# Kernel tuning notes

Hardware: AMD Instinct MI355X
Metric: run time of the kernel (lower is better)

Reference implementation:

```python
import jax, jax.numpy as jnp
import numpy as np

N_NODES = 50000; N_INTRA = 800000; N_INTER = 400000; N_IEDGE = 600000
N_GRAPHS = 128; F_IN = 54; DIM = 128; N_GNN = 3; DIM_MLP = 128
DEV_VDW_COEFF = 0.2; EPS_LO = 0.0178; EPS_HI = 0.2
VDW_N_SHORT = 10.0; VDW_N_LONG = 6.0
RANGE_LO = 0.5; RANGE_HI = 5.0
HBOND_CUT = (-0.7, 0.0); METAL_CUT = (-0.7, 0.0); HYDRO_CUT = (0.5, 1.5)


def _lin(key, fi, fo):
    return jax.random.normal(key, (fi, fo), jnp.float32) / np.float32(np.sqrt(fi))


def setup_inputs():
    key = jax.random.key(0)
    ks = iter(jax.random.split(key, 48))
    nk = lambda: next(ks)
    inp = {}
    inp['x'] = jax.random.normal(nk(), (N_NODES, F_IN), jnp.float32)
    inp['pos'] = jax.random.uniform(nk(), (N_NODES, 3), jnp.float32, 0.0, 20.0)
    inp['vdw_radii'] = jax.random.uniform(nk(), (N_NODES,), jnp.float32, 1.0, 2.0)
    inp['rotor'] = jax.random.randint(nk(), (N_GRAPHS, 1), 0, 20).astype(jnp.float32)
    inp['edge_index'] = jax.random.randint(nk(), (2, N_INTRA), 0, N_NODES)
    inp['edge_index_c'] = jax.random.randint(nk(), (2, N_INTER), 0, N_NODES)
    inp['edge_index_i'] = jax.random.randint(nk(), (2, N_IEDGE), 0, N_NODES)
    inp['batch'] = jnp.sort(jax.random.randint(nk(), (N_NODES,), 0, N_GRAPHS))
    for name, p in (('is_metal', 0.02), ('is_h_donor', 0.15), ('is_h_acceptor', 0.2), ('is_hydrophobic', 0.4)):
        inp[name] = jax.random.bernoulli(nk(), p, (N_NODES,))
    inp['embed_W'] = _lin(nk(), F_IN, DIM)
    inp['gat_W'] = jax.random.normal(nk(), (N_GNN, DIM, DIM), jnp.float32) / np.float32(np.sqrt(DIM))
    inp['gat_Wb'] = jnp.zeros((N_GNN, DIM), jnp.float32)
    inp['gat_A'] = 0.1 * jax.random.normal(nk(), (N_GNN, DIM, DIM), jnp.float32) / np.float32(np.sqrt(DIM))
    inp['gat_gate_w'] = jax.random.normal(nk(), (N_GNN, 2 * DIM, 1), jnp.float32) / np.float32(np.sqrt(2 * DIM))
    inp['gat_gate_b'] = jnp.zeros((N_GNN, 1), jnp.float32)
    inp['inter_W'] = jax.random.normal(nk(), (N_GNN, DIM, DIM), jnp.float32) / np.float32(np.sqrt(DIM))
    inp['inter_Wb'] = jnp.zeros((N_GNN, DIM), jnp.float32)
    inp['inter_gate_w'] = jax.random.normal(nk(), (N_GNN, 2 * DIM, 1), jnp.float32) / np.float32(np.sqrt(2 * DIM))
    inp['inter_gate_b'] = jnp.zeros((N_GNN, 1), jnp.float32)
    inp['eps_w1'] = _lin(nk(), 2 * DIM, DIM_MLP); inp['eps_b1'] = jnp.zeros((DIM_MLP,), jnp.float32)
    inp['eps_w2'] = _lin(nk(), DIM_MLP, 1); inp['eps_b2'] = jnp.zeros((1,), jnp.float32)
    inp['dvdw_w1'] = _lin(nk(), 2 * DIM, DIM_MLP); inp['dvdw_b1'] = jnp.zeros((DIM_MLP,), jnp.float32)
    inp['dvdw_w2'] = _lin(nk(), DIM_MLP, 1); inp['dvdw_b2'] = jnp.zeros((1,), jnp.float32)
    inp['hbond_coeff'] = jnp.array([1.0], jnp.float32)
    inp['hydrophobic_coeff'] = jnp.array([0.5], jnp.float32)
    inp['rotor_coeff'] = jnp.array([0.5], jnp.float32)
    return inp


def _gated_gat(x, src, dst, W, Wb, A, gw, gb):
    n = x.shape[0]
    h = x @ W + Wb                                   # [N, D]
    logits = jnp.sum((h @ A)[dst] * h[src], axis=-1)  # per-edge attention logit
    mx = jax.ops.segment_max(logits, dst, num_segments=n)
    mx = jnp.where(jnp.isfinite(mx), mx, 0.0)
    ex = jnp.exp(logits - mx[dst])
    den = jax.ops.segment_sum(ex, dst, num_segments=n)
    alpha = ex / (den[dst] + 1e-16)                  # segment softmax over incoming edges
    h_prime = jax.nn.relu(jax.ops.segment_sum(alpha[:, None] * h[src], dst, num_segments=n))
    z = jax.nn.sigmoid(jnp.concatenate([x, h_prime], -1) @ gw + gb)
    return z * x + (1.0 - z) * h_prime


def _interaction(x, src, dst, W, Wb, gw, gb):
    n = x.shape[0]
    m = jax.ops.segment_sum(jax.nn.relu(x[src] @ W + Wb), dst, num_segments=n)
    z = jax.nn.sigmoid(jnp.concatenate([x, m], -1) @ gw + gb)
    return z * x + (1.0 - z) * m


def _lj(D, R, eps, n_short, n_long):
    dr = jnp.maximum(D / R, 0.5)  # numerical clamp mirroring PIGNet's distance clamp
    n = jnp.where(dr < 1.0, n_short, n_long)
    return eps * (dr ** (-2.0 * n) - 2.0 * dr ** (-n))


def _linear_potential(D, R, minima, c_short, c_long):
    frac = jnp.clip(((D - R) - c_long) / (c_short - c_long), 0.0, 1.0)
    return minima * frac


def _forward(x, pos, vdw_radii, rotor, embed_W, gat_W, gat_Wb, gat_A, gat_gate_w, gat_gate_b,
             inter_W, inter_Wb, inter_gate_w, inter_gate_b,
             eps_w1, eps_b1, eps_w2, eps_b2, dvdw_w1, dvdw_b1, dvdw_w2, dvdw_b2,
             hbond_coeff, hydrophobic_coeff, rotor_coeff,
             edge_index, edge_index_c, edge_index_i, batch,
             is_metal, is_h_donor, is_h_acceptor, is_hydrophobic):
    h = x @ embed_W
    for l in range(N_GNN):
        h = _gated_gat(h, edge_index[0], edge_index[1], gat_W[l], gat_Wb[l], gat_A[l], gat_gate_w[l], gat_gate_b[l])
    for l in range(N_GNN):
        h = _interaction(h, edge_index_c[0], edge_index_c[1], inter_W[l], inter_Wb[l], inter_gate_w[l], inter_gate_b[l])
    i, j = edge_index_i[0], edge_index_i[1]
    diff = pos[i] - pos[j]
    D = jnp.sqrt(jnp.sum(diff * diff, axis=-1) + 1e-10)           # [E]
    rmask = ((D >= RANGE_LO) & (D <= RANGE_HI)).astype(h.dtype)
    x_cat = jnp.concatenate([h[i], h[j]], axis=-1)                # [E, 2*DIM]
    dvdw = jnp.tanh(jax.nn.relu(x_cat @ dvdw_w1 + dvdw_b1) @ dvdw_w2 + dvdw_b2)[:, 0]
    dvdw = dvdw * DEV_VDW_COEFF * rmask
    R = vdw_radii[i] + vdw_radii[j] + dvdw
    eps = jax.nn.sigmoid(jax.nn.relu(x_cat @ eps_w1 + eps_b1) @ eps_w2 + eps_b2)[:, 0]
    eps = eps * (EPS_HI - EPS_LO) + EPS_LO
    min_hb = -hbond_coeff ** 2
    min_hp = -hydrophobic_coeff ** 2
    e = jnp.stack([
        _lj(D, R, eps, VDW_N_SHORT, VDW_N_LONG),
        _linear_potential(D, R, min_hb, *HBOND_CUT),
        _linear_potential(D, R, min_hb, *METAL_CUT),
        _linear_potential(D, R, min_hp, *HYDRO_CUT),
    ])                                                            # [4, E]
    no_metal = ~(is_metal[i] | is_metal[j])
    masks = jnp.stack([
        no_metal,
        ((is_h_donor[i] & is_h_acceptor[j]) | (is_h_acceptor[i] & is_h_donor[j])) & no_metal,
        (is_metal[i] & is_h_acceptor[j]) | (is_h_acceptor[i] & is_metal[j]),
        is_hydrophobic[i] & is_hydrophobic[j] & no_metal,
    ]).astype(e.dtype)
    e = e * masks * rmask
    energies = jax.ops.segment_sum(e.T, batch[i], num_segments=N_GRAPHS)  # [G, 4]
    penalty = 1.0 + rotor_coeff ** 2 * rotor                               # [G, 1]
    return energies / penalty, dvdw


def reference(x, pos, vdw_radii, rotor, edge_index, edge_index_c, edge_index_i, batch,
              is_metal, is_h_donor, is_h_acceptor, is_hydrophobic,
              embed_W, gat_W, gat_Wb, gat_A, gat_gate_w, gat_gate_b,
              inter_W, inter_Wb, inter_gate_w, inter_gate_b,
              eps_w1, eps_b1, eps_w2, eps_b2, dvdw_w1, dvdw_b1, dvdw_w2, dvdw_b2,
              hbond_coeff, hydrophobic_coeff, rotor_coeff):
    return _forward(x, pos, vdw_radii, rotor, embed_W, gat_W, gat_Wb, gat_A, gat_gate_w, gat_gate_b,
                    inter_W, inter_Wb, inter_gate_w, inter_gate_b,
                    eps_w1, eps_b1, eps_w2, eps_b2, dvdw_w1, dvdw_b1, dvdw_w2, dvdw_b2,
                    hbond_coeff, hydrophobic_coeff, rotor_coeff,
                    edge_index, edge_index_c, edge_index_i, batch,
                    is_metal, is_h_donor, is_h_acceptor, is_hydrophobic)
```

## Files before the change

### kernel.cpp

```cpp
#include <hip/hip_runtime.h>
#include <math.h>

#define NN 50000
#define EA 800000
#define EC 400000
#define EIN 600000
#define NG 128
#define FIN 54

#define DEV_VDW 0.2f
#define EPS_LO_ 0.0178f
#define EPS_HI_ 0.2f

typedef unsigned int uint;
typedef unsigned short ushort;
typedef __attribute__((ext_vector_type(8))) short bf16x8;
typedef __attribute__((ext_vector_type(4))) float f32x4;

__device__ __forceinline__ ushort f2bf(float f){
  uint x = __float_as_uint(f);
  uint r = x + 0x7fffu + ((x >> 16) & 1u);
  return (ushort)(r >> 16);
}
__device__ __forceinline__ uint f2bf2(float a, float b){
  return (uint)f2bf(a) | ((uint)f2bf(b) << 16);
}
__device__ __forceinline__ float2 bf2x2(uint u){
  return make_float2(__uint_as_float(u << 16), __uint_as_float(u & 0xffff0000u));
}
__device__ __forceinline__ void decode8(uint4 u, float* f){
  f[0] = __uint_as_float(u.x << 16); f[1] = __uint_as_float(u.x & 0xffff0000u);
  f[2] = __uint_as_float(u.y << 16); f[3] = __uint_as_float(u.y & 0xffff0000u);
  f[4] = __uint_as_float(u.z << 16); f[5] = __uint_as_float(u.z & 0xffff0000u);
  f[6] = __uint_as_float(u.w << 16); f[7] = __uint_as_float(u.w & 0xffff0000u);
}

__global__ void k_count(const int* __restrict__ dst, int E, int* __restrict__ cnt){
  int i = blockIdx.x * blockDim.x + threadIdx.x;
  int stride = gridDim.x * blockDim.x;
  for (; i < E; i += stride) atomicAdd(&cnt[dst[i]], 1);
}

__global__ void k_scan(const int* __restrict__ cnt, int n, int* __restrict__ off, int* __restrict__ cur){
  __shared__ int wsums[16];
  __shared__ int run_s;
  int tid = threadIdx.x;
  int lane = tid & 63, w = tid >> 6;
  if (tid == 0) run_s = 0;
  __syncthreads();
  for (int base = 0; base < n; base += 1024){
    int run = run_s;
    int i = base + tid;
    int v = (i < n) ? cnt[i] : 0;
    int s = v;
    #pragma unroll
    for (int o = 1; o < 64; o <<= 1){ int t = __shfl_up(s, o, 64); if (lane >= o) s += t; }
    if (lane == 63) wsums[w] = s;
    __syncthreads();
    if (w == 0 && lane < 16){
      int t = wsums[lane];
      #pragma unroll
      for (int o = 1; o < 16; o <<= 1){ int u = __shfl_up(t, o, 64); if (lane >= o) t += u; }
      wsums[lane] = t;
    }
    __syncthreads();
    int woff = (w == 0) ? 0 : wsums[w - 1];
    int excl = run + woff + (s - v);
    if (i < n){ off[i] = excl; cur[i] = excl; }
    int tot = wsums[15];
    __syncthreads();
    if (tid == 0) run_s = run + tot;
    __syncthreads();
  }
  if (threadIdx.x == 0) off[n] = run_s;
}

__global__ void k_place(const int* __restrict__ src, const int* __restrict__ dst, int E,
                        int* __restrict__ cur, int* __restrict__ out_src){
  int i = blockIdx.x * blockDim.x + threadIdx.x;
  int stride = gridDim.x * blockDim.x;
  for (; i < E; i += stride){
    int d = dst[i];
    int slot = atomicAdd(&cur[d], 1);
    out_src[slot] = src[i];
  }
}

__global__ void k_nodeinfo(const float* __restrict__ POS, const float* __restrict__ RAD,
                           const int* __restrict__ Mmet, const int* __restrict__ Mdon,
                           const int* __restrict__ Macc, const int* __restrict__ Mhyd,
                           const int* __restrict__ BATCH,
                           float4* __restrict__ PRAD, uint* __restrict__ MB){
  int n = blockIdx.x * 256 + threadIdx.x;
  if (n < NN){
    PRAD[n] = make_float4(POS[3*n], POS[3*n+1], POS[3*n+2], RAD[n]);
    uint m = (Mmet[n] ? 1u : 0u) | (Mdon[n] ? 2u : 0u) | (Macc[n] ? 4u : 0u) |
             (Mhyd[n] ? 8u : 0u) | ((uint)BATCH[n] << 8);
    MB[n] = m;
  }
}

__global__ __launch_bounds__(256) void k_prepw(const float* __restrict__ gatW, const float* __restrict__ gatA,
                        const float* __restrict__ intW, const float* __restrict__ dw1,
                        const float* __restrict__ ew1, const float* __restrict__ db1,
                        const float* __restrict__ eb1,
                        uint* __restrict__ Wt, float* __restrict__ BIASB){
  __shared__ ushort L[128 * 130];
  int m = blockIdx.x;
  int tid = threadIdx.x;
  if (m == 13){
    if (tid < 512){
      int c = tid & 127, y = tid >> 7;
      float v = (y == 0) ? db1[c] : (y == 2) ? eb1[c] : 0.f;
      BIASB[tid] = v;
    }
    if (tid < 128) BIASB[512 + tid] = 0.f;
    return;
  }
  const float* src = (m < 3)  ? gatW + m * 16384 :
                     (m < 6)  ? gatA + (m - 3) * 16384 :
                     (m < 9)  ? intW + (m - 6) * 16384 :
                     (m < 11) ? dw1 + (m - 9) * 16384 :
                                ew1 + (m - 11) * 16384;
  for (int idx = tid; idx < 16384; idx += 256){
    int k = idx >> 7, n = idx & 127;
    L[k * 130 + n] = f2bf(src[idx]);
  }
  __syncthreads();
  int n = tid & 127, half = tid >> 7;
  uint* outp = Wt + (size_t)m * 8192 + n * 64 + half * 32;
  #pragma unroll
  for (int kk2 = 0; kk2 < 32; ++kk2){
    int k = half * 64 + 2 * kk2;
    uint u = (uint)L[k * 130 + n] | ((uint)L[(k + 1) * 130 + n] << 16);
    outp[kk2] = u;
  }
}

__global__ void k_embed(const float* __restrict__ X, const float* __restrict__ W,
                        float* __restrict__ H, uint* __restrict__ Hh){
  __shared__ float Wls[FIN * 128];
  int tid = threadIdx.x;
  for (int i = tid; i < FIN * 128; i += 128) Wls[i] = W[i];
  __syncthreads();
  for (int row = blockIdx.x; row < NN; row += gridDim.x){
    const float* xr = X + row * FIN;
    float acc = 0.f;
    #pragma unroll
    for (int k = 0; k < FIN; ++k) acc += xr[k] * Wls[k * 128 + tid];
    H[(size_t)row * 128 + tid] = acc;
    ((ushort*)Hh)[(size_t)row * 128 + tid] = f2bf(acc);
  }
}

template<bool RELU>
__global__ __launch_bounds__(256) void k_gemm_mfma(const uint* __restrict__ Ah,
        const uint* __restrict__ Bt0, const float* __restrict__ bias0,
        uint* __restrict__ C0, size_t strideC, int N){
  const uint* Bt = Bt0 + (size_t)blockIdx.y * 8192;
  const float* bias = bias0 + (size_t)blockIdx.y * 128;
  uint* Cout = C0 + (size_t)blockIdx.y * strideC;
  int tid = threadIdx.x;
  int lane = tid & 63;
  int wv = tid >> 6;
  int row0 = blockIdx.x * 128 + wv * 32;
  int l15 = lane & 15, lg = lane >> 4;
  int ra0 = row0 + l15, ra1 = row0 + 16 + l15;
  const uint* pa0 = Ah + (size_t)(ra0 < N ? ra0 : 0) * 64 + lg * 4;
  const uint* pa1 = Ah + (size_t)(ra1 < N ? ra1 : 0) * 64 + lg * 4;
  const uint* pb  = Bt + (size_t)l15 * 64 + lg * 4;
  f32x4 acc[2][8] = {};
  #pragma unroll
  for (int c = 0; c < 4; ++c){
    bf16x8 a0 = *(const bf16x8*)(pa0 + c * 16);
    bf16x8 a1 = *(const bf16x8*)(pa1 + c * 16);
    #pragma unroll
    for (int ct = 0; ct < 8; ++ct){
      bf16x8 b = *(const bf16x8*)(pb + ct * 1024 + c * 16);
      acc[0][ct] = __builtin_amdgcn_mfma_f32_16x16x32_bf16(a0, b, acc[0][ct], 0, 0, 0);
      acc[1][ct] = __builtin_amdgcn_mfma_f32_16x16x32_bf16(a1, b, acc[1][ct], 0, 0, 0);
    }
  }
  #pragma unroll
  for (int ct = 0; ct < 8; ++ct){
    int col = ct * 16 + l15;
    float bv = bias[col];
    #pragma unroll
    for (int rt = 0; rt < 2; ++rt){
      int rbase = row0 + rt * 16 + lg * 4;
      f32x4 a4 = acc[rt][ct];
      #pragma unroll
      for (int r = 0; r < 4; ++r){
        int row = rbase + r;
        if (row < N){
          float t = a4[r] + bv;
          if (RELU) t = fmaxf(t, 0.f);
          ((ushort*)Cout)[(size_t)row * 128 + col] = f2bf(t);
        }
      }
    }
  }
}

__global__ __launch_bounds__(256) void k_gat(float* __restrict__ H, uint* __restrict__ Hh,
                      const uint* __restrict__ HWh, const uint* __restrict__ HAh,
                      const int* __restrict__ off, const int* __restrict__ srcs,
                      const float* __restrict__ GW, const float* __restrict__ GB){
  int tid = threadIdx.x;
  int sub = tid & 15;
  int n = blockIdx.x * 16 + (tid >> 4);
  if (n >= NN) return;
  uint4 au = *(const uint4*)(HAh + (size_t)n * 64 + sub * 4);
  float a[8]; decode8(au, a);
  int e0 = off[n], deg = off[n + 1] - e0;
  float m = -INFINITY, den = 0.f;
  float acc[8] = {};
  uint4 wu = {};
  if (deg > 0){
    int s = srcs[e0];
    wu = *(const uint4*)(HWh + (size_t)s * 64 + sub * 4);
  }
  for (int t = 0; t < deg; ++t){
    uint4 wnow = wu;
    if (t + 1 < deg){
      int s2 = srcs[e0 + t + 1];
      wu = *(const uint4*)(HWh + (size_t)s2 * 64 + sub * 4);
    }
    float w[8]; decode8(wnow, w);
    float p = a[0]*w[0] + a[1]*w[1] + a[2]*w[2] + a[3]*w[3]
            + a[4]*w[4] + a[5]*w[5] + a[6]*w[6] + a[7]*w[7];
    #pragma unroll
    for (int o = 8; o; o >>= 1) p += __shfl_xor(p, o, 64);
    float mn = fmaxf(m, p);
    float cf = __expf(m - mn);
    float ex = __expf(p - mn);
    den = den * cf + ex;
    #pragma unroll
    for (int q = 0; q < 8; ++q) acc[q] = acc[q] * cf + ex * w[q];
    m = mn;
  }
  float inv = 1.f / (den + 1e-16f);
  float hp[8];
  #pragma unroll
  for (int q = 0; q < 8; ++q) hp[q] = fmaxf(acc[q] * inv, 0.f);
  float x[8];
  *(float4*)&x[0] = *(const float4*)(H + (size_t)n * 128 + sub * 8);
  *(float4*)&x[4] = *(const float4*)(H + (size_t)n * 128 + sub * 8 + 4);
  float gx[8], gh[8];
  *(float4*)&gx[0] = *(const float4*)(GW + sub * 8);
  *(float4*)&gx[4] = *(const float4*)(GW + sub * 8 + 4);
  *(float4*)&gh[0] = *(const float4*)(GW + 128 + sub * 8);
  *(float4*)&gh[4] = *(const float4*)(GW + 128 + sub * 8 + 4);
  float g = 0.f;
  #pragma unroll
  for (int q = 0; q < 8; ++q) g += x[q] * gx[q] + hp[q] * gh[q];
  #pragma unroll
  for (int o = 8; o; o >>= 1) g += __shfl_xor(g, o, 64);
  g += GB[0];
  float z = 1.f / (1.f + __expf(-g));
  #pragma unroll
  for (int q = 0; q < 8; ++q) x[q] = z * x[q] + (1.f - z) * hp[q];
  *(float4*)(H + (size_t)n * 128 + sub * 8)     = *(float4*)&x[0];
  *(float4*)(H + (size_t)n * 128 + sub * 8 + 4) = *(float4*)&x[4];
  uint4 hw;
  hw.x = f2bf2(x[0], x[1]); hw.y = f2bf2(x[2], x[3]);
  hw.z = f2bf2(x[4], x[5]); hw.w = f2bf2(x[6], x[7]);
  *(uint4*)(Hh + (size_t)n * 64 + sub * 4) = hw;
}

__global__ __launch_bounds__(256) void k_inter(float* __restrict__ H, uint* __restrict__ Hh,
                        const uint* __restrict__ Th,
                        const int* __restrict__ off, const int* __restrict__ srcs,
                        const float* __restrict__ GW, const float* __restrict__ GB){
  int tid = threadIdx.x;
  int sub = tid & 15;
  int n = blockIdx.x * 16 + (tid >> 4);
  if (n >= NN) return;
  int e0 = off[n], deg = off[n + 1] - e0;
  float acc[8] = {};
  uint4 wu = {};
  if (deg > 0){
    int s = srcs[e0];
    wu = *(const uint4*)(Th + (size_t)s * 64 + sub * 4);
  }
  for (int t = 0; t < deg; ++t){
    uint4 wnow = wu;
    if (t + 1 < deg){
      int s2 = srcs[e0 + t + 1];
      wu = *(const uint4*)(Th + (size_t)s2 * 64 + sub * 4);
    }
    float w[8]; decode8(wnow, w);
    #pragma unroll
    for (int q = 0; q < 8; ++q) acc[q] += w[q];
  }
  float x[8];
  *(float4*)&x[0] = *(const float4*)(H + (size_t)n * 128 + sub * 8);
  *(float4*)&x[4] = *(const float4*)(H + (size_t)n * 128 + sub * 8 + 4);
  float gx[8], gh[8];
  *(float4*)&gx[0] = *(const float4*)(GW + sub * 8);
  *(float4*)&gx[4] = *(const float4*)(GW + sub * 8 + 4);
  *(float4*)&gh[0] = *(const float4*)(GW + 128 + sub * 8);
  *(float4*)&gh[4] = *(const float4*)(GW + 128 + sub * 8 + 4);
  float g = 0.f;
  #pragma unroll
  for (int q = 0; q < 8; ++q) g += x[q] * gx[q] + acc[q] * gh[q];
  #pragma unroll
  for (int o = 8; o; o >>= 1) g += __shfl_xor(g, o, 64);
  g += GB[0];
  float z = 1.f / (1.f + __expf(-g));
  #pragma unroll
  for (int q = 0; q < 8; ++q) x[q] = z * x[q] + (1.f - z) * acc[q];
  *(float4*)(H + (size_t)n * 128 + sub * 8)     = *(float4*)&x[0];
  *(float4*)(H + (size_t)n * 128 + sub * 8 + 4) = *(float4*)&x[4];
  uint4 hw;
  hw.x = f2bf2(x[0], x[1]); hw.y = f2bf2(x[2], x[3]);
  hw.z = f2bf2(x[4], x[5]); hw.w = f2bf2(x[6], x[7]);
  *(uint4*)(Hh + (size_t)n * 64 + sub * 4) = hw;
}

__global__ __launch_bounds__(256) void k_edges(
    const int* __restrict__ EI,
    const float4* __restrict__ PRAD, const uint* __restrict__ MB,
    const uint* __restrict__ Pd, const uint* __restrict__ Qd,
    const uint* __restrict__ Pe, const uint* __restrict__ Qe,
    const float* __restrict__ w2d, const float* __restrict__ b2d,
    const float* __restrict__ w2e, const float* __restrict__ b2e,
    const float* __restrict__ hbc, const float* __restrict__ hpc,
    float* __restrict__ geng, float* __restrict__ outdv){
  __shared__ float eg[NG * 4];
  int tid = threadIdx.x;
  for (int i = tid; i < NG * 4; i += 256) eg[i] = 0.f;
  __syncthreads();
  int sub = tid & 15;
  int gid = blockIdx.x * 16 + (tid >> 4);
  int ngrp = gridDim.x * 16;
  float wdv[8], wev[8];
  *(float4*)&wdv[0] = *(const float4*)(w2d + sub * 8);
  *(float4*)&wdv[4] = *(const float4*)(w2d + sub * 8 + 4);
  *(float4*)&wev[0] = *(const float4*)(w2e + sub * 8);
  *(float4*)&wev[4] = *(const float4*)(w2e + sub * 8 + 4);
  float bd = b2d[0], be = b2e[0];
  float minhb = -hbc[0] * hbc[0], minhp = -hpc[0] * hpc[0];

  int e = gid;
  uint4 pd0 = {}, qd0 = {}, pe0 = {}, qe0 = {};
  float4 pri0 = {}, prj0 = {};
  uint mbi0 = 0, mbj0 = 0;
  int i1 = 0, j1 = 0;
  if (e < EIN){
    int i0 = EI[e], j0 = EI[EIN + e];
    pd0 = *(const uint4*)(Pd + (size_t)i0 * 64 + sub * 4);
    qd0 = *(const uint4*)(Qd + (size_t)j0 * 64 + sub * 4);
    pe0 = *(const uint4*)(Pe + (size_t)i0 * 64 + sub * 4);
    qe0 = *(const uint4*)(Qe + (size_t)j0 * 64 + sub * 4);
    pri0 = PRAD[i0]; prj0 = PRAD[j0]; mbi0 = MB[i0]; mbj0 = MB[j0];
  }
  if (e + ngrp < EIN){ i1 = EI[e + ngrp]; j1 = EI[EIN + e + ngrp]; }

  for (; e < EIN; e += ngrp){
    uint4 pd1 = {}, qd1 = {}, pe1 = {}, qe1 = {};
    float4 pri1 = {}, prj1 = {};
    uint mbi1 = 0, mbj1 = 0;
    int i2 = 0, j2 = 0;
    if (e + ngrp < EIN){
      pd1 = *(const uint4*)(Pd + (size_t)i1 * 64 + sub * 4);
      qd1 = *(const uint4*)(Qd + (size_t)j1 * 64 + sub * 4);
      pe1 = *(const uint4*)(Pe + (size_t)i1 * 64 + sub * 4);
      qe1 = *(const uint4*)(Qe + (size_t)j1 * 64 + sub * 4);
      pri1 = PRAD[i1]; prj1 = PRAD[j1]; mbi1 = MB[i1]; mbj1 = MB[j1];
    }
    if (e + 2 * ngrp < EIN){ i2 = EI[e + 2 * ngrp]; j2 = EI[EIN + e + 2 * ngrp]; }

    float pdf[8], qdf[8], pef[8], qef[8];
    decode8(pd0, pdf); decode8(qd0, qdf); decode8(pe0, pef); decode8(qe0, qef);
    float sd = 0.f, se = 0.f;
    #pragma unroll
    for (int q = 0; q < 8; ++q){
      sd += fmaxf(pdf[q] + qdf[q], 0.f) * wdv[q];
      se += fmaxf(pef[q] + qef[q], 0.f) * wev[q];
    }
    #pragma unroll
    for (int o = 8; o; o >>= 1){
      sd += __shfl_xor(sd, o, 64);
      se += __shfl_xor(se, o, 64);
    }
    sd += bd; se += be;
    float dx = pri0.x - prj0.x, dy = pri0.y - prj0.y, dz = pri0.z - prj0.z;
    float D = sqrtf(dx * dx + dy * dy + dz * dz + 1e-10f);
    float rmask = (D >= 0.5f && D <= 5.0f) ? 1.f : 0.f;
    float dvdw = tanhf(sd) * DEV_VDW * rmask;
    float eps = (1.f / (1.f + __expf(-se))) * (EPS_HI_ - EPS_LO_) + EPS_LO_;
    float R = pri0.w + prj0.w + dvdw;
    float dr = fmaxf(D / R, 0.5f);
    float nn2 = (dr < 1.f) ? 10.f : 6.f;
    float tp = __expf(-nn2 * __logf(dr));
    float ev = eps * (tp * tp - 2.f * tp);
    float dmr = D - R;
    float f1 = fminf(fmaxf(dmr * (-1.f / 0.7f), 0.f), 1.f);
    float f3 = fminf(fmaxf(1.5f - dmr, 0.f), 1.f);
    bool metI = mbi0 & 1, metJ = mbj0 & 1;
    bool donI = mbi0 & 2, donJ = mbj0 & 2;
    bool accI = mbi0 & 4, accJ = mbj0 & 4;
    bool hyI  = mbi0 & 8, hyJ  = mbj0 & 8;
    bool nm = !(metI || metJ);
    float E0 = nm ? ev * rmask : 0.f;
    float E1 = (((donI && accJ) || (accI && donJ)) && nm) ? minhb * f1 * rmask : 0.f;
    float E2 = ((metI && accJ) || (accI && metJ)) ? minhb * f1 * rmask : 0.f;
    float E3 = (hyI && hyJ && nm) ? minhp * f3 * rmask : 0.f;
    if (sub == 0){
      outdv[e] = dvdw;
      int g = (int)(mbi0 >> 8) * 4;
      atomicAdd(&eg[g + 0], E0);
      atomicAdd(&eg[g + 1], E1);
      atomicAdd(&eg[g + 2], E2);
      atomicAdd(&eg[g + 3], E3);
    }
    pd0 = pd1; qd0 = qd1; pe0 = pe1; qe0 = qe1;
    pri0 = pri1; prj0 = prj1; mbi0 = mbi1; mbj0 = mbj1;
    i1 = i2; j1 = j2;
  }
  __syncthreads();
  float* part = geng + (size_t)(blockIdx.x & 7) * (NG * 4);
  for (int i2 = tid; i2 < NG * 4; i2 += 256) atomicAdd(&part[i2], eg[i2]);
}

__global__ void k_final(const float* __restrict__ geng, const float* __restrict__ rotor,
                        const float* __restrict__ rc, float* __restrict__ out){
  int t = blockIdx.x * blockDim.x + threadIdx.x;
  if (t < NG * 4){
    int g = t >> 2;
    float s = 0.f;
    #pragma unroll
    for (int p = 0; p < 8; ++p) s += geng[p * NG * 4 + t];
    float pen = 1.f + rc[0] * rc[0] * rotor[g];
    out[t] = s / pen;
  }
}

extern "C" void kernel_launch(void* const* d_in, const int* in_sizes, int n_in,
                              void* d_out, int out_size, void* d_ws, size_t ws_size,
                              hipStream_t stream){
  (void)in_sizes; (void)n_in; (void)out_size; (void)ws_size;
  const float* X    = (const float*)d_in[0];
  const float* POS  = (const float*)d_in[1];
  const float* RAD  = (const float*)d_in[2];
  const float* ROT  = (const float*)d_in[3];
  const int* EIa    = (const int*)d_in[4];
  const int* EIc    = (const int*)d_in[5];
  const int* EIi    = (const int*)d_in[6];
  const int* BATCH  = (const int*)d_in[7];
  const int* Mmet = (const int*)d_in[8];
  const int* Mdon = (const int*)d_in[9];
  const int* Macc = (const int*)d_in[10];
  const int* Mhyd = (const int*)d_in[11];
  const float* embW  = (const float*)d_in[12];
  const float* gatW  = (const float*)d_in[13];
  const float* gatWb = (const float*)d_in[14];
  const float* gatA  = (const float*)d_in[15];
  const float* gatGw = (const float*)d_in[16];
  const float* gatGb = (const float*)d_in[17];
  const float* intW  = (const float*)d_in[18];
  const float* intWb = (const float*)d_in[19];
  const float* intGw = (const float*)d_in[20];
  const float* intGb = (const float*)d_in[21];
  const float* ew1 = (const float*)d_in[22];
  const float* eb1 = (const float*)d_in[23];
  const float* ew2 = (const float*)d_in[24];
  const float* eb2 = (const float*)d_in[25];
  const float* dw1 = (const float*)d_in[26];
  const float* db1 = (const float*)d_in[27];
  const float* dw2 = (const float*)d_in[28];
  const float* db2 = (const float*)d_in[29];
  const float* hbc = (const float*)d_in[30];
  const float* hpc = (const float*)d_in[31];
  const float* rcc = (const float*)d_in[32];
  float* out = (float*)d_out;

  char* w = (char*)d_ws;
  float* H   = (float*)w; w += (size_t)NN * 128 * 4;
  uint* Hh   = (uint*)w;  w += (size_t)NN * 64 * 4;
  uint* BAh  = (uint*)w;  w += (size_t)NN * 64 * 4;
  uint* BBh  = (uint*)w;  w += (size_t)NN * 64 * 4;
  uint* Peh  = (uint*)w;  w += (size_t)NN * 64 * 4;
  uint* Qeh  = (uint*)w;  w += (size_t)NN * 64 * 4;
  uint* WT   = (uint*)w;  w += (size_t)13 * 8192 * 4;
  float* BIASB = (float*)w; w += 640 * 4;
  float4* PRAD = (float4*)w; w += (size_t)NN * 16;
  uint* MBb  = (uint*)w;  w += (size_t)NN * 4;
  float* GENG = (float*)w; w += (size_t)8 * 512 * 4;
  int* cntA = (int*)w; w += (size_t)NN * 4;
  int* offA = (int*)w; w += (size_t)(NN + 1) * 4;
  int* curA = (int*)w; w += (size_t)NN * 4;
  int* srcA = (int*)w; w += (size_t)EA * 4;
  int* cntC = (int*)w; w += (size_t)NN * 4;
  int* offC = (int*)w; w += (size_t)(NN + 1) * 4;
  int* curC = (int*)w; w += (size_t)NN * 4;
  int* srcC = (int*)w; w += (size_t)EC * 4;
  uint* Th  = BAh;
  uint* Pdh = BAh;
  uint* Qdh = BBh;
  const float* zeros128 = BIASB + 512;

  hipMemsetAsync(cntA, 0, (size_t)NN * 4, stream);
  hipMemsetAsync(cntC, 0, (size_t)NN * 4, stream);
  hipMemsetAsync(GENG, 0, (size_t)8 * 512 * 4, stream);

  k_count<<<1024, 256, 0, stream>>>(EIa + EA, EA, cntA);
  k_scan<<<1, 1024, 0, stream>>>(cntA, NN, offA, curA);
  k_place<<<1024, 256, 0, stream>>>(EIa, EIa + EA, EA, curA, srcA);
  k_count<<<1024, 256, 0, stream>>>(EIc + EC, EC, cntC);
  k_scan<<<1, 1024, 0, stream>>>(cntC, NN, offC, curC);
  k_place<<<1024, 256, 0, stream>>>(EIc, EIc + EC, EC, curC, srcC);

  k_prepw<<<14, 256, 0, stream>>>(gatW, gatA, intW, dw1, ew1, db1, eb1, WT, BIASB);
  k_nodeinfo<<<(NN + 255) / 256, 256, 0, stream>>>(POS, RAD, Mmet, Mdon, Macc, Mhyd, BATCH, PRAD, MBb);
  k_embed<<<2048, 128, 0, stream>>>(X, embW, H, Hh);

  int gg = (NN + 127) / 128;
  int nodeGrid = (NN + 15) / 16;
  for (int l = 0; l < 3; ++l){
    k_gemm_mfma<false><<<dim3(gg, 1), 256, 0, stream>>>(Hh,  WT + (size_t)l * 8192,       gatWb + l * 128, BAh, 0, NN);
    k_gemm_mfma<false><<<dim3(gg, 1), 256, 0, stream>>>(BAh, WT + (size_t)(3 + l) * 8192, zeros128,        BBh, 0, NN);
    k_gat<<<nodeGrid, 256, 0, stream>>>(H, Hh, BAh, BBh, offA, srcA, gatGw + l * 256, gatGb + l);
  }
  for (int l = 0; l < 3; ++l){
    k_gemm_mfma<true><<<dim3(gg, 1), 256, 0, stream>>>(Hh, WT + (size_t)(6 + l) * 8192, intWb + l * 128, Th, 0, NN);
    k_inter<<<nodeGrid, 256, 0, stream>>>(H, Hh, Th, offC, srcC, intGw + l * 256, intGb + l);
  }
  k_gemm_mfma<false><<<dim3(gg, 4), 256, 0, stream>>>(Hh, WT + (size_t)9 * 8192, BIASB, BAh, (size_t)NN * 64, NN);

  k_edges<<<2048, 256, 0, stream>>>(EIi, PRAD, MBb, Pdh, Qdh, Peh, Qeh,
                                    dw2, db2, ew2, eb2, hbc, hpc,
                                    GENG, out + 512);
  k_final<<<2, 256, 0, stream>>>(GENG, ROT, rcc, out);
}
```

Measured before the change: 852.8 us.

## Precompose GAT weight products, split neighbor loops across lanes, merge CSR builds

Several changes at once. The GAT attention matrix is folded into the layer weight at prep time (A' = W·A, plus bias·A), so the two chained GEMMs per layer become a single GEMM launch with two outputs. The GAT and inter aggregation kernels now use a 64-lane wave per node, with four lane groups each taking every fourth neighbor; the partial online-softmax results and the sums are merged with shuffles, which adds parallelism for memory-latency-bound gathers. The A and C CSR count/scan/place kernels are merged into single launches, and the edge kernel uses fast tanh and division intrinsics. The precomposed weight is rounded to bf16 after the product rather than before the second GEMM, which changes numerics slightly.

```diff
diff --git a/kernel.cpp b/kernel.cpp
--- a/kernel.cpp
+++ b/kernel.cpp
@@ -25,9 +25,6 @@
 __device__ __forceinline__ uint f2bf2(float a, float b){
   return (uint)f2bf(a) | ((uint)f2bf(b) << 16);
 }
-__device__ __forceinline__ float2 bf2x2(uint u){
-  return make_float2(__uint_as_float(u << 16), __uint_as_float(u & 0xffff0000u));
-}
 __device__ __forceinline__ void decode8(uint4 u, float* f){
   f[0] = __uint_as_float(u.x << 16); f[1] = __uint_as_float(u.x & 0xffff0000u);
   f[2] = __uint_as_float(u.y << 16); f[3] = __uint_as_float(u.y & 0xffff0000u);
@@ -35,13 +32,23 @@
   f[6] = __uint_as_float(u.w << 16); f[7] = __uint_as_float(u.w & 0xffff0000u);
 }
 
-__global__ void k_count(const int* __restrict__ dst, int E, int* __restrict__ cnt){
-  int i = blockIdx.x * blockDim.x + threadIdx.x;
-  int stride = gridDim.x * blockDim.x;
-  for (; i < E; i += stride) atomicAdd(&cnt[dst[i]], 1);
-}
-
-__global__ void k_scan(const int* __restrict__ cnt, int n, int* __restrict__ off, int* __restrict__ cur){
+__global__ void k_count2(const int* __restrict__ dstA, const int* __restrict__ dstC,
+                         int* __restrict__ cntA, int* __restrict__ cntC){
+  int half = blockIdx.x >= 1024;
+  const int* dst = half ? dstC : dstA;
+  int* cnt = half ? cntC : cntA;
+  int E = half ? EC : EA;
+  int bid = blockIdx.x - (half ? 1024 : 0);
+  int i = bid * 256 + threadIdx.x;
+  for (; i < E; i += 1024 * 256) atomicAdd(&cnt[dst[i]], 1);
+}
+
+__global__ void k_scan2(const int* __restrict__ cntA, int* __restrict__ offA, int* __restrict__ curA,
+                        const int* __restrict__ cntC, int* __restrict__ offC, int* __restrict__ curC){
+  const int* cnt = blockIdx.x ? cntC : cntA;
+  int* off = blockIdx.x ? offC : offA;
+  int* cur = blockIdx.x ? curC : curA;
+  int n = NN;
   __shared__ int wsums[16];
   __shared__ int run_s;
   int tid = threadIdx.x;
@@ -75,14 +82,21 @@
   if (threadIdx.x == 0) off[n] = run_s;
 }
 
-__global__ void k_place(const int* __restrict__ src, const int* __restrict__ dst, int E,
-                        int* __restrict__ cur, int* __restrict__ out_src){
-  int i = blockIdx.x * blockDim.x + threadIdx.x;
-  int stride = gridDim.x * blockDim.x;
-  for (; i < E; i += stride){
+__global__ void k_place2(const int* __restrict__ eiA, const int* __restrict__ eiC,
+                         int* __restrict__ curA, int* __restrict__ srcA,
+                         int* __restrict__ curC, int* __restrict__ srcC){
+  int half = blockIdx.x >= 1024;
+  const int* src = half ? eiC : eiA;
+  const int* dst = half ? eiC + EC : eiA + EA;
+  int* cur = half ? curC : curA;
+  int* outp = half ? srcC : srcA;
+  int E = half ? EC : EA;
+  int bid = blockIdx.x - (half ? 1024 : 0);
+  int i = bid * 256 + threadIdx.x;
+  for (; i < E; i += 1024 * 256){
     int d = dst[i];
     int slot = atomicAdd(&cur[d], 1);
-    out_src[slot] = src[i];
+    outp[slot] = src[i];
   }
 }
 
@@ -102,29 +116,75 @@
 
 __global__ __launch_bounds__(256) void k_prepw(const float* __restrict__ gatW, const float* __restrict__ gatA,
                         const float* __restrict__ intW, const float* __restrict__ dw1,
-                        const float* __restrict__ ew1, const float* __restrict__ db1,
-                        const float* __restrict__ eb1,
-                        uint* __restrict__ Wt, float* __restrict__ BIASB){
-  __shared__ ushort L[128 * 130];
+                        const float* __restrict__ ew1,
+                        const float* __restrict__ gatWb, const float* __restrict__ intWb,
+                        const float* __restrict__ db1, const float* __restrict__ eb1,
+                        uint* __restrict__ Wt, float* __restrict__ BIASALL){
+  __shared__ ushort L[128 * 132];
   int m = blockIdx.x;
   int tid = threadIdx.x;
   if (m == 13){
-    if (tid < 512){
-      int c = tid & 127, y = tid >> 7;
-      float v = (y == 0) ? db1[c] : (y == 2) ? eb1[c] : 0.f;
-      BIASB[tid] = v;
-    }
-    if (tid < 128) BIASB[512 + tid] = 0.f;
+    for (int idx = tid; idx < 13 * 128; idx += 256){
+      int slot = idx >> 7, c = idx & 127;
+      if (slot >= 3 && slot < 6) continue;
+      float v = 0.f;
+      if (slot < 3) v = gatWb[slot * 128 + c];
+      else if (slot < 9) v = intWb[(slot - 6) * 128 + c];
+      else if (slot == 9) v = db1[c];
+      else if (slot == 11) v = eb1[c];
+      BIASALL[idx] = v;
+    }
     return;
   }
+  if (m >= 3 && m < 6){
+    int l = m - 3;
+    const float* Wf  = gatW + l * 16384;
+    const float* Af  = gatA + l * 16384;
+    const float* Wbf = gatWb + l * 128;
+    for (int idx = tid; idx < 16384; idx += 256){
+      int k = idx >> 7, n = idx & 127;
+      L[k * 132 + n] = f2bf(Af[idx]);
+    }
+    __syncthreads();
+    int r = tid >> 1, ch = tid & 1;
+    float accv[64];
+    #pragma unroll
+    for (int c = 0; c < 64; ++c) accv[c] = 0.f;
+    float accb = 0.f;
+    int bc = tid & 127;
+    for (int mm = 0; mm < 128; ++mm){
+      float wv = Wf[r * 128 + mm];
+      const uint* Lr32 = (const uint*)&L[mm * 132 + ch * 64];
+      #pragma unroll
+      for (int c2 = 0; c2 < 32; ++c2){
+        uint u = Lr32[c2];
+        accv[2 * c2]     += wv * __uint_as_float(u << 16);
+        accv[2 * c2 + 1] += wv * __uint_as_float(u & 0xffff0000u);
+      }
+      accb += Wbf[mm] * __uint_as_float((uint)L[mm * 132 + bc] << 16);
+    }
+    __syncthreads();
+    #pragma unroll
+    for (int c = 0; c < 64; ++c) L[r * 132 + ch * 64 + c] = f2bf(accv[c]);
+    if (tid < 128) BIASALL[(3 + l) * 128 + tid] = accb;
+    __syncthreads();
+    int n = tid & 127, half = tid >> 7;
+    uint* outp = Wt + (size_t)m * 8192 + n * 64 + half * 32;
+    #pragma unroll
+    for (int kk2 = 0; kk2 < 32; ++kk2){
+      int k = half * 64 + 2 * kk2;
+      uint u = (uint)L[k * 132 + n] | ((uint)L[(k + 1) * 132 + n] << 16);
+      outp[kk2] = u;
+    }
+    return;
+  }
   const float* src = (m < 3)  ? gatW + m * 16384 :
-                     (m < 6)  ? gatA + (m - 3) * 16384 :
                      (m < 9)  ? intW + (m - 6) * 16384 :
                      (m < 11) ? dw1 + (m - 9) * 16384 :
                                 ew1 + (m - 11) * 16384;
   for (int idx = tid; idx < 16384; idx += 256){
     int k = idx >> 7, n = idx & 127;
-    L[k * 130 + n] = f2bf(src[idx]);
+    L[k * 132 + n] = f2bf(src[idx]);
   }
   __syncthreads();
   int n = tid & 127, half = tid >> 7;
@@ -132,7 +192,7 @@
   #pragma unroll
   for (int kk2 = 0; kk2 < 32; ++kk2){
     int k = half * 64 + 2 * kk2;
-    uint u = (uint)L[k * 130 + n] | ((uint)L[(k + 1) * 130 + n] << 16);
+    uint u = (uint)L[k * 132 + n] | ((uint)L[(k + 1) * 132 + n] << 16);
     outp[kk2] = u;
   }
 }
@@ -155,10 +215,11 @@
 
 template<bool RELU>
 __global__ __launch_bounds__(256) void k_gemm_mfma(const uint* __restrict__ Ah,
-        const uint* __restrict__ Bt0, const float* __restrict__ bias0,
+        const uint* __restrict__ Bt0, size_t strideB,
+        const float* __restrict__ bias0, size_t strideBias,
         uint* __restrict__ C0, size_t strideC, int N){
-  const uint* Bt = Bt0 + (size_t)blockIdx.y * 8192;
-  const float* bias = bias0 + (size_t)blockIdx.y * 128;
+  const uint* Bt = Bt0 + (size_t)blockIdx.y * strideB;
+  const float* bias = bias0 + (size_t)blockIdx.y * strideBias;
   uint* Cout = C0 + (size_t)blockIdx.y * strideC;
   int tid = threadIdx.x;
   int lane = tid & 63;
@@ -207,36 +268,58 @@
                       const int* __restrict__ off, const int* __restrict__ srcs,
                       const float* __restrict__ GW, const float* __restrict__ GB){
   int tid = threadIdx.x;
-  int sub = tid & 15;
-  int n = blockIdx.x * 16 + (tid >> 4);
+  int n = blockIdx.x * 4 + (tid >> 6);
   if (n >= NN) return;
+  int lane = tid & 63;
+  int sub = lane & 15;
+  int grp = lane >> 4;
   uint4 au = *(const uint4*)(HAh + (size_t)n * 64 + sub * 4);
   float a[8]; decode8(au, a);
   int e0 = off[n], deg = off[n + 1] - e0;
-  float m = -INFINITY, den = 0.f;
+  float m = -1e30f, den = 0.f;
   float acc[8] = {};
+  int slot = grp;
+  bool act = slot < deg;
+  int sv = (sub == 0 && act) ? srcs[e0 + slot] : 0;
+  int s = __shfl(sv, lane & 48);
   uint4 wu = {};
-  if (deg > 0){
-    int s = srcs[e0];
-    wu = *(const uint4*)(HWh + (size_t)s * 64 + sub * 4);
-  }
-  for (int t = 0; t < deg; ++t){
-    uint4 wnow = wu;
-    if (t + 1 < deg){
-      int s2 = srcs[e0 + t + 1];
-      wu = *(const uint4*)(HWh + (size_t)s2 * 64 + sub * 4);
-    }
-    float w[8]; decode8(wnow, w);
+  if (act) wu = *(const uint4*)(HWh + (size_t)s * 64 + sub * 4);
+  int nit = (deg + 3) >> 2;
+  for (int t = 0; t < nit; ++t){
+    int slotn = slot + 4;
+    bool actn = slotn < deg;
+    int svn = (sub == 0 && actn) ? srcs[e0 + slotn] : 0;
+    int sn = __shfl(svn, lane & 48);
+    uint4 wun = {};
+    if (actn) wun = *(const uint4*)(HWh + (size_t)sn * 64 + sub * 4);
+    float w[8]; decode8(wu, w);
     float p = a[0]*w[0] + a[1]*w[1] + a[2]*w[2] + a[3]*w[3]
             + a[4]*w[4] + a[5]*w[5] + a[6]*w[6] + a[7]*w[7];
     #pragma unroll
     for (int o = 8; o; o >>= 1) p += __shfl_xor(p, o, 64);
-    float mn = fmaxf(m, p);
-    float cf = __expf(m - mn);
-    float ex = __expf(p - mn);
-    den = den * cf + ex;
-    #pragma unroll
-    for (int q = 0; q < 8; ++q) acc[q] = acc[q] * cf + ex * w[q];
+    if (act){
+      float mn = fmaxf(m, p);
+      float cf = __expf(m - mn);
+      float ex = __expf(p - mn);
+      den = den * cf + ex;
+      #pragma unroll
+      for (int q = 0; q < 8; ++q) acc[q] = acc[q] * cf + ex * w[q];
+      m = mn;
+    }
+    slot = slotn; act = actn; wu = wun;
+  }
+  #pragma unroll
+  for (int o = 16; o <= 32; o <<= 1){
+    float mo  = __shfl_xor(m, o, 64);
+    float dno = __shfl_xor(den, o, 64);
+    float ao[8];
+    #pragma unroll
+    for (int q = 0; q < 8; ++q) ao[q] = __shfl_xor(acc[q], o, 64);
+    float mn = fmaxf(m, mo);
+    float cf = __expf(m - mn), cfo = __expf(mo - mn);
+    den = den * cf + dno * cfo;
+    #pragma unroll
+    for (int q = 0; q < 8; ++q) acc[q] = acc[q] * cf + ao[q] * cfo;
     m = mn;
   }
   float inv = 1.f / (den + 1e-16f);
@@ -260,12 +343,14 @@
   float z = 1.f / (1.f + __expf(-g));
   #pragma unroll
   for (int q = 0; q < 8; ++q) x[q] = z * x[q] + (1.f - z) * hp[q];
-  *(float4*)(H + (size_t)n * 128 + sub * 8)     = *(float4*)&x[0];
-  *(float4*)(H + (size_t)n * 128 + sub * 8 + 4) = *(float4*)&x[4];
-  uint4 hw;
-  hw.x = f2bf2(x[0], x[1]); hw.y = f2bf2(x[2], x[3]);
-  hw.z = f2bf2(x[4], x[5]); hw.w = f2bf2(x[6], x[7]);
-  *(uint4*)(Hh + (size_t)n * 64 + sub * 4) = hw;
+  if (grp == 0){
+    *(float4*)(H + (size_t)n * 128 + sub * 8)     = *(float4*)&x[0];
+    *(float4*)(H + (size_t)n * 128 + sub * 8 + 4) = *(float4*)&x[4];
+    uint4 hw;
+    hw.x = f2bf2(x[0], x[1]); hw.y = f2bf2(x[2], x[3]);
+    hw.z = f2bf2(x[4], x[5]); hw.w = f2bf2(x[6], x[7]);
+    *(uint4*)(Hh + (size_t)n * 64 + sub * 4) = hw;
+  }
 }
 
 __global__ __launch_bounds__(256) void k_inter(float* __restrict__ H, uint* __restrict__ Hh,
@@ -273,25 +358,38 @@
                         const int* __restrict__ off, const int* __restrict__ srcs,
                         const float* __restrict__ GW, const float* __restrict__ GB){
   int tid = threadIdx.x;
-  int sub = tid & 15;
-  int n = blockIdx.x * 16 + (tid >> 4);
+  int n = blockIdx.x * 4 + (tid >> 6);
   if (n >= NN) return;
+  int lane = tid & 63;
+  int sub = lane & 15;
+  int grp = lane >> 4;
   int e0 = off[n], deg = off[n + 1] - e0;
   float acc[8] = {};
+  int slot = grp;
+  bool act = slot < deg;
+  int sv = (sub == 0 && act) ? srcs[e0 + slot] : 0;
+  int s = __shfl(sv, lane & 48);
   uint4 wu = {};
-  if (deg > 0){
-    int s = srcs[e0];
-    wu = *(const uint4*)(Th + (size_t)s * 64 + sub * 4);
-  }
-  for (int t = 0; t < deg; ++t){
-    uint4 wnow = wu;
-    if (t + 1 < deg){
-      int s2 = srcs[e0 + t + 1];
-      wu = *(const uint4*)(Th + (size_t)s2 * 64 + sub * 4);
-    }
-    float w[8]; decode8(wnow, w);
-    #pragma unroll
-    for (int q = 0; q < 8; ++q) acc[q] += w[q];
+  if (act) wu = *(const uint4*)(Th + (size_t)s * 64 + sub * 4);
+  int nit = (deg + 3) >> 2;
+  for (int t = 0; t < nit; ++t){
+    int slotn = slot + 4;
+    bool actn = slotn < deg;
+    int svn = (sub == 0 && actn) ? srcs[e0 + slotn] : 0;
+    int sn = __shfl(svn, lane & 48);
+    uint4 wun = {};
+    if (actn) wun = *(const uint4*)(Th + (size_t)sn * 64 + sub * 4);
+    if (act){
+      float w[8]; decode8(wu, w);
+      #pragma unroll
+      for (int q = 0; q < 8; ++q) acc[q] += w[q];
+    }
+    slot = slotn; act = actn; wu = wun;
+  }
+  #pragma unroll
+  for (int q = 0; q < 8; ++q){
+    acc[q] += __shfl_xor(acc[q], 16, 64);
+    acc[q] += __shfl_xor(acc[q], 32, 64);
   }
   float x[8];
   *(float4*)&x[0] = *(const float4*)(H + (size_t)n * 128 + sub * 8);
@@ -310,12 +408,14 @@
   float z = 1.f / (1.f + __expf(-g));
   #pragma unroll
   for (int q = 0; q < 8; ++q) x[q] = z * x[q] + (1.f - z) * acc[q];
-  *(float4*)(H + (size_t)n * 128 + sub * 8)     = *(float4*)&x[0];
-  *(float4*)(H + (size_t)n * 128 + sub * 8 + 4) = *(float4*)&x[4];
-  uint4 hw;
-  hw.x = f2bf2(x[0], x[1]); hw.y = f2bf2(x[2], x[3]);
-  hw.z = f2bf2(x[4], x[5]); hw.w = f2bf2(x[6], x[7]);
-  *(uint4*)(Hh + (size_t)n * 64 + sub * 4) = hw;
+  if (grp == 0){
+    *(float4*)(H + (size_t)n * 128 + sub * 8)     = *(float4*)&x[0];
+    *(float4*)(H + (size_t)n * 128 + sub * 8 + 4) = *(float4*)&x[4];
+    uint4 hw;
+    hw.x = f2bf2(x[0], x[1]); hw.y = f2bf2(x[2], x[3]);
+    hw.z = f2bf2(x[4], x[5]); hw.w = f2bf2(x[6], x[7]);
+    *(uint4*)(Hh + (size_t)n * 64 + sub * 4) = hw;
+  }
 }
 
 __global__ __launch_bounds__(256) void k_edges(
@@ -388,10 +488,12 @@
     float dx = pri0.x - prj0.x, dy = pri0.y - prj0.y, dz = pri0.z - prj0.z;
     float D = sqrtf(dx * dx + dy * dy + dz * dz + 1e-10f);
     float rmask = (D >= 0.5f && D <= 5.0f) ? 1.f : 0.f;
-    float dvdw = tanhf(sd) * DEV_VDW * rmask;
-    float eps = (1.f / (1.f + __expf(-se))) * (EPS_HI_ - EPS_LO_) + EPS_LO_;
+    float ex2 = __expf(2.f * fminf(sd, 15.f));
+    float th = __fdividef(ex2 - 1.f, ex2 + 1.f);
+    float dvdw = th * DEV_VDW * rmask;
+    float eps = __fdividef(1.f, 1.f + __expf(-se)) * (EPS_HI_ - EPS_LO_) + EPS_LO_;
     float R = pri0.w + prj0.w + dvdw;
-    float dr = fmaxf(D / R, 0.5f);
+    float dr = fmaxf(__fdividef(D, R), 0.5f);
     float nn2 = (dr < 1.f) ? 10.f : 6.f;
     float tp = __expf(-nn2 * __logf(dr));
     float ev = eps * (tp * tp - 2.f * tp);
@@ -484,7 +586,7 @@
   uint* Peh  = (uint*)w;  w += (size_t)NN * 64 * 4;
   uint* Qeh  = (uint*)w;  w += (size_t)NN * 64 * 4;
   uint* WT   = (uint*)w;  w += (size_t)13 * 8192 * 4;
-  float* BIASB = (float*)w; w += 640 * 4;
+  float* BIASALL = (float*)w; w += (size_t)13 * 128 * 4;
   float4* PRAD = (float4*)w; w += (size_t)NN * 16;
   uint* MBb  = (uint*)w;  w += (size_t)NN * 4;
   float* GENG = (float*)w; w += (size_t)8 * 512 * 4;
@@ -499,35 +601,35 @@
   uint* Th  = BAh;
   uint* Pdh = BAh;
   uint* Qdh = BBh;
-  const float* zeros128 = BIASB + 512;
 
   hipMemsetAsync(cntA, 0, (size_t)NN * 4, stream);
   hipMemsetAsync(cntC, 0, (size_t)NN * 4, stream);
   hipMemsetAsync(GENG, 0, (size_t)8 * 512 * 4, stream);
 
-  k_count<<<1024, 256, 0, stream>>>(EIa + EA, EA, cntA);
-  k_scan<<<1, 1024, 0, stream>>>(cntA, NN, offA, curA);
-  k_place<<<1024, 256, 0, stream>>>(EIa, EIa + EA, EA, curA, srcA);
-  k_count<<<1024, 256, 0, stream>>>(EIc + EC, EC, cntC);
-  k_scan<<<1, 1024, 0, stream>>>(cntC, NN, offC, curC);
-  k_place<<<1024, 256, 0, stream>>>(EIc, EIc + EC, EC, curC, srcC);
-
-  k_prepw<<<14, 256, 0, stream>>>(gatW, gatA, intW, dw1, ew1, db1, eb1, WT, BIASB);
+  k_count2<<<2048, 256, 0, stream>>>(EIa + EA, EIc + EC, cntA, cntC);
+  k_scan2<<<2, 1024, 0, stream>>>(cntA, offA, curA, cntC, offC, curC);
+  k_place2<<<2048, 256, 0, stream>>>(EIa, EIc, curA, srcA, curC, srcC);
+
+  k_prepw<<<14, 256, 0, stream>>>(gatW, gatA, intW, dw1, ew1, gatWb, intWb, db1, eb1, WT, BIASALL);
   k_nodeinfo<<<(NN + 255) / 256, 256, 0, stream>>>(POS, RAD, Mmet, Mdon, Macc, Mhyd, BATCH, PRAD, MBb);
   k_embed<<<2048, 128, 0, stream>>>(X, embW, H, Hh);
 
   int gg = (NN + 127) / 128;
-  int nodeGrid = (NN + 15) / 16;
+  int nodeGrid = (NN + 3) / 4;
   for (int l = 0; l < 3; ++l){
-    k_gemm_mfma<false><<<dim3(gg, 1), 256, 0, stream>>>(Hh,  WT + (size_t)l * 8192,       gatWb + l * 128, BAh, 0, NN);
-    k_gemm_mfma<false><<<dim3(gg, 1), 256, 0, stream>>>(BAh, WT + (size_t)(3 + l) * 8192, zeros128,        BBh, 0, NN);
+    k_gemm_mfma<false><<<dim3(gg, 2), 256, 0, stream>>>(Hh, WT + (size_t)l * 8192, (size_t)3 * 8192,
+                                                        BIASALL + l * 128, (size_t)3 * 128,
+                                                        BAh, (size_t)NN * 64, NN);
     k_gat<<<nodeGrid, 256, 0, stream>>>(H, Hh, BAh, BBh, offA, srcA, gatGw + l * 256, gatGb + l);
   }
   for (int l = 0; l < 3; ++l){
-    k_gemm_mfma<true><<<dim3(gg, 1), 256, 0, stream>>>(Hh, WT + (size_t)(6 + l) * 8192, intWb + l * 128, Th, 0, NN);
+    k_gemm_mfma<true><<<dim3(gg, 1), 256, 0, stream>>>(Hh, WT + (size_t)(6 + l) * 8192, 0,
+                                                       BIASALL + (6 + l) * 128, 0, Th, 0, NN);
     k_inter<<<nodeGrid, 256, 0, stream>>>(H, Hh, Th, offC, srcC, intGw + l * 256, intGb + l);
   }
-  k_gemm_mfma<false><<<dim3(gg, 4), 256, 0, stream>>>(Hh, WT + (size_t)9 * 8192, BIASB, BAh, (size_t)NN * 64, NN);
+  k_gemm_mfma<false><<<dim3(gg, 4), 256, 0, stream>>>(Hh, WT + (size_t)9 * 8192, (size_t)8192,
+                                                      BIASALL + 9 * 128, (size_t)128,
+                                                      BAh, (size_t)NN * 64, NN);
 
   k_edges<<<2048, 256, 0, stream>>>(EIi, PRAD, MBb, Pdh, Qdh, Peh, Qeh,
                                     dw2, db2, ew2, eb2, hbc, hpc,
```

New measurement: 894.0 us. +4.8%, slower.
